# Kernel optimization log

Hardware: AMD Instinct MI355X
Metric: run time of the kernel (lower is better)

## Reference

```python
import jax, jax.numpy as jnp
import numpy as np

B, T, C = 2, 4096, 768
H = 12
D = C // H  # head_dim = 64


def setup_inputs() -> dict:
    key = jax.random.key(0)
    kx, kq, kk, kv, ko = jax.random.split(key, 5)
    s = 1.0 / np.sqrt(C)  # keep activations well-scaled
    return {
        "x": jax.random.normal(kx, (B, T, C), dtype=jnp.float32),
        "wq": jax.random.normal(kq, (C, C), dtype=jnp.float32) * s,
        "wk": jax.random.normal(kk, (C, C), dtype=jnp.float32) * s,
        "wv": jax.random.normal(kv, (C, C), dtype=jnp.float32) * s,
        "wo": jax.random.normal(ko, (C, C), dtype=jnp.float32) * s,
    }


def reference(x, wq, wk, wv, wo):
    b, t, c = x.shape
    # projections (torch Linear: y = x @ W.T); split heads -> (B,H,T,D)
    q = (x @ wq.T).reshape(b, t, H, D).transpose(0, 2, 1, 3)
    k = (x @ wk.T).reshape(b, t, H, D).transpose(0, 2, 1, 3)
    v = (x @ wv.T).reshape(b, t, H, D).transpose(0, 2, 1, 3)
    scale = 1.0 / jnp.sqrt(jnp.asarray(D, dtype=x.dtype))
    scores = jnp.einsum("bhqd,bhkd->bhqk", q, k) * scale  # (B,H,T,T)
    causal = jnp.tril(jnp.ones((t, t), dtype=bool))
    scores = jnp.where(causal, scores, jnp.asarray(-jnp.inf, dtype=scores.dtype))
    attn = jax.nn.softmax(scores, axis=-1)
    ctx = jnp.einsum("bhqk,bhkd->bhqd", attn, v)  # (B,H,T,D)
    ctx = ctx.transpose(0, 2, 1, 3).reshape(b, t, c)
    return ctx @ wo.T
```

## Files before the change

kernel.cpp:

```cpp
#include <hip/hip_runtime.h>
#include <hip/hip_bf16.h>

#define B_  2
#define T_  4096
#define C_  768
#define H_  12
#define D_  64
#define MTOT (B_*T_)

typedef __bf16 bf16;
typedef __bf16 bf16x8 __attribute__((ext_vector_type(8)));
typedef __bf16 bf16x4 __attribute__((ext_vector_type(4)));
typedef float  f32x4  __attribute__((ext_vector_type(4)));

__device__ __forceinline__ void gl_lds16(const bf16* g, bf16* l) {
    __builtin_amdgcn_global_load_lds(
        (const __attribute__((address_space(1))) void*)g,
        (__attribute__((address_space(3))) void*)l, 16, 0, 0);
}

__global__ __launch_bounds__(256) void cvt_bf16(const float* __restrict__ src,
                                                bf16* __restrict__ dst, int n8) {
    int i = blockIdx.x * 256 + threadIdx.x;
    if (i >= n8) return;
    const float4* s4 = (const float4*)src;
    float4 a = s4[2*(size_t)i], b = s4[2*(size_t)i+1];
    bf16x8 o;
    o[0]=(bf16)a.x; o[1]=(bf16)a.y; o[2]=(bf16)a.z; o[3]=(bf16)a.w;
    o[4]=(bf16)b.x; o[5]=(bf16)b.y; o[6]=(bf16)b.z; o[7]=(bf16)b.w;
    *(bf16x8*)(dst + 8*(size_t)i) = o;
}

__global__ __launch_bounds__(256) void cvt_bf16_w4(const float* __restrict__ w0,
                                                   const float* __restrict__ w1,
                                                   const float* __restrict__ w2,
                                                   const float* __restrict__ w3,
                                                   bf16* __restrict__ d0,
                                                   bf16* __restrict__ d1,
                                                   bf16* __restrict__ d2,
                                                   bf16* __restrict__ d3) {
    int z = blockIdx.y;
    const float* src = (z==0)?w0:(z==1)?w1:(z==2)?w2:w3;
    bf16* dst = (z==0)?d0:(z==1)?d1:(z==2)?d2:d3;
    int i = blockIdx.x * 256 + threadIdx.x;
    const float4* s4 = (const float4*)src;
    float4 a = s4[2*(size_t)i], b = s4[2*(size_t)i+1];
    bf16x8 o;
    o[0]=(bf16)a.x; o[1]=(bf16)a.y; o[2]=(bf16)a.z; o[3]=(bf16)a.w;
    o[4]=(bf16)b.x; o[5]=(bf16)b.y; o[6]=(bf16)b.z; o[7]=(bf16)b.w;
    *(bf16x8*)(dst + 8*(size_t)i) = o;
}

__global__ __launch_bounds__(256) void gemm_qkv(const bf16* __restrict__ xb,
                                                const bf16* __restrict__ wqb,
                                                const bf16* __restrict__ wkb,
                                                const bf16* __restrict__ wvb,
                                                bf16* __restrict__ qo,
                                                bf16* __restrict__ ko,
                                                bf16* __restrict__ vto) {
    int z = blockIdx.z;
    const bf16* w = (z == 0) ? wqb : (z == 1) ? wkb : wvb;
    bf16* dst = (z == 0) ? qo : (z == 1) ? ko : vto;
    int mbase = blockIdx.x * 128;
    int nbase = blockIdx.y * 128;
    __shared__ bf16 As[128][32];
    __shared__ bf16 Bs[128][32];
    int tid  = threadIdx.x;
    int wave = tid >> 6, lane = tid & 63;
    int wm = (wave >> 1) * 64, wn = (wave & 1) * 64;
    int lr = lane & 15, lg = lane >> 4;
    int srow0 = tid >> 2, scol0 = tid & 3;
    int srow1 = (tid + 256) >> 2, scol1 = (tid + 256) & 3;
    f32x4 acc[4][4] = {};
    for (int kb = 0; kb < C_; kb += 32) {
        gl_lds16(xb + (size_t)(mbase + srow0) * C_ + kb + scol0 * 8, &As[srow0][scol0 * 8]);
        gl_lds16(xb + (size_t)(mbase + srow1) * C_ + kb + scol1 * 8, &As[srow1][scol1 * 8]);
        gl_lds16(w  + (size_t)(nbase + srow0) * C_ + kb + scol0 * 8, &Bs[srow0][scol0 * 8]);
        gl_lds16(w  + (size_t)(nbase + srow1) * C_ + kb + scol1 * 8, &Bs[srow1][scol1 * 8]);
        __syncthreads();
        bf16x8 af[4], bfr[4];
        #pragma unroll
        for (int mt = 0; mt < 4; ++mt) af[mt]  = *(const bf16x8*)(&As[wm + mt*16 + lr][lg*8]);
        #pragma unroll
        for (int nt = 0; nt < 4; ++nt) bfr[nt] = *(const bf16x8*)(&Bs[wn + nt*16 + lr][lg*8]);
        #pragma unroll
        for (int mt = 0; mt < 4; ++mt)
            #pragma unroll
            for (int nt = 0; nt < 4; ++nt)
                acc[mt][nt] = __builtin_amdgcn_mfma_f32_16x16x32_bf16(af[mt], bfr[nt], acc[mt][nt], 0, 0, 0);
        __syncthreads();
    }
    float sc = (z == 0) ? 0.18033688011112042f : 1.0f;
    int m0 = mbase + wm + (lg << 2);
    int n0 = nbase + wn + lr;
    if (z < 2) {
        #pragma unroll
        for (int mt = 0; mt < 4; ++mt) {
            #pragma unroll
            for (int nt = 0; nt < 4; ++nt) {
                int n = n0 + nt * 16;
                int h = n >> 6, d = n & 63;
                #pragma unroll
                for (int r = 0; r < 4; ++r) {
                    int m = m0 + mt * 16 + r;
                    int b = m >> 12, t = m & 4095;
                    dst[(((size_t)b * H_ + h) * T_ + t) * 64 + d] = (bf16)(acc[mt][nt][r] * sc);
                }
            }
        }
    } else {
        #pragma unroll
        for (int mt = 0; mt < 4; ++mt) {
            int m = m0 + mt * 16;
            int b = m >> 12, t = m & 4095;
            #pragma unroll
            for (int nt = 0; nt < 4; ++nt) {
                int n = n0 + nt * 16;
                int h = n >> 6, d = n & 63;
                bf16x4 pk;
                #pragma unroll
                for (int r = 0; r < 4; ++r) pk[r] = (bf16)acc[mt][nt][r];
                *(bf16x4*)(dst + (((size_t)b * H_ + h) * 64 + d) * T_ + t) = pk;
            }
        }
    }
}

__global__ __launch_bounds__(256) void gemm_out(const bf16* __restrict__ ctx,
                                                const bf16* __restrict__ wob,
                                                float* __restrict__ out) {
    int mbase = blockIdx.x * 128;
    int nbase = blockIdx.y * 128;
    __shared__ bf16 As[128][32];
    __shared__ bf16 Bs[128][32];
    int tid  = threadIdx.x;
    int wave = tid >> 6, lane = tid & 63;
    int wm = (wave >> 1) * 64, wn = (wave & 1) * 64;
    int lr = lane & 15, lg = lane >> 4;
    int srow0 = tid >> 2, scol0 = tid & 3;
    int srow1 = (tid + 256) >> 2, scol1 = (tid + 256) & 3;
    f32x4 acc[4][4] = {};
    for (int kb = 0; kb < C_; kb += 32) {
        gl_lds16(ctx + (size_t)(mbase + srow0) * C_ + kb + scol0 * 8, &As[srow0][scol0 * 8]);
        gl_lds16(ctx + (size_t)(mbase + srow1) * C_ + kb + scol1 * 8, &As[srow1][scol1 * 8]);
        gl_lds16(wob + (size_t)(nbase + srow0) * C_ + kb + scol0 * 8, &Bs[srow0][scol0 * 8]);
        gl_lds16(wob + (size_t)(nbase + srow1) * C_ + kb + scol1 * 8, &Bs[srow1][scol1 * 8]);
        __syncthreads();
        bf16x8 af[4], bfr[4];
        #pragma unroll
        for (int mt = 0; mt < 4; ++mt) af[mt]  = *(const bf16x8*)(&As[wm + mt*16 + lr][lg*8]);
        #pragma unroll
        for (int nt = 0; nt < 4; ++nt) bfr[nt] = *(const bf16x8*)(&Bs[wn + nt*16 + lr][lg*8]);
        #pragma unroll
        for (int mt = 0; mt < 4; ++mt)
            #pragma unroll
            for (int nt = 0; nt < 4; ++nt)
                acc[mt][nt] = __builtin_amdgcn_mfma_f32_16x16x32_bf16(af[mt], bfr[nt], acc[mt][nt], 0, 0, 0);
        __syncthreads();
    }
    int m0 = mbase + wm + (lg << 2);
    int n0 = nbase + wn + lr;
    #pragma unroll
    for (int mt = 0; mt < 4; ++mt)
        #pragma unroll
        for (int nt = 0; nt < 4; ++nt)
            #pragma unroll
            for (int r = 0; r < 4; ++r)
                out[(size_t)(m0 + mt * 16 + r) * C_ + n0 + nt * 16] = acc[mt][nt][r];
}

__global__ __launch_bounds__(256, 4) void attn(const bf16* __restrict__ q,
                                               const bf16* __restrict__ k,
                                               const bf16* __restrict__ vt,
                                               bf16* __restrict__ ctx) {
    int idx = blockIdx.x;
    int qt = 63 - idx / 24;
    int bh = idx % 24;
    int b = bh / H_, h = bh % H_;
    int tid = threadIdx.x;
    int wave = tid >> 6, lane = tid & 63;
    int lr = lane & 15, lg = lane >> 4;

    __shared__ bf16 Ks[64][72];
    __shared__ bf16 Vs[64][72];
    __shared__ bf16 Pb[4][16][72];

    const bf16* qp = q  + (size_t)bh * T_ * 64;
    const bf16* kp = k  + (size_t)bh * T_ * 64;
    const bf16* vp = vt + (size_t)bh * 64 * (size_t)T_;

    int r0 = tid >> 3, c0 = tid & 7;
    const bf16* kstg = kp + (size_t)r0 * 64 + c0 * 8;
    const bf16* vstg = vp + (size_t)r0 * T_ + c0 * 8;

    const float NEGINF = -__builtin_inff();

    int qb = qt * 64 + wave * 16;
    int n  = qt + 1;
    int qrow = qb + lr;

    bf16x8 qf[2];
    #pragma unroll
    for (int c = 0; c < 2; ++c)
        qf[c] = *(const bf16x8*)(qp + (size_t)(qb + lr) * 64 + c * 32 + lg * 8);

    f32x4 o[4] = {};
    float m = NEGINF, l = 0.f;

    uint4 sk0 = *(const uint4*)(kstg);
    uint4 sk1 = *(const uint4*)(kstg + 32 * 64);
    uint4 sv0 = *(const uint4*)(vstg);
    uint4 sv1 = *(const uint4*)(vstg + (size_t)32 * T_);

    for (int kb = 0; kb < n; ++kb) {
        int kv = kb * 64;
        __syncthreads();
        *(uint4*)(&Ks[r0][c0 * 8])      = sk0;
        *(uint4*)(&Ks[32 + r0][c0 * 8]) = sk1;
        *(uint4*)(&Vs[r0][c0 * 8])      = sv0;
        *(uint4*)(&Vs[32 + r0][c0 * 8]) = sv1;
        if (kb + 1 < n) {
            const bf16* ksrc = kstg + (size_t)(kb + 1) * 64 * 64;
            const bf16* vsrc = vstg + (size_t)(kb + 1) * 64;
            sk0 = *(const uint4*)(ksrc);
            sk1 = *(const uint4*)(ksrc + 32 * 64);
            sv0 = *(const uint4*)(vsrc);
            sv1 = *(const uint4*)(vsrc + (size_t)32 * T_);
        }
        __syncthreads();

        f32x4 s[4] = {};
        #pragma unroll
        for (int c2 = 0; c2 < 2; ++c2)
            #pragma unroll
            for (int nt = 0; nt < 4; ++nt) {
                bf16x8 kf = *(const bf16x8*)(&Ks[nt * 16 + lr][c2 * 32 + lg * 8]);
                s[nt] = __builtin_amdgcn_mfma_f32_16x16x32_bf16(kf, qf[c2], s[nt], 0, 0, 0);
            }
        if (kb == qt) {
            #pragma unroll
            for (int nt = 0; nt < 4; ++nt)
                #pragma unroll
                for (int r = 0; r < 4; ++r) {
                    int key = kv + nt * 16 + lg * 4 + r;
                    s[nt][r] = (key > qrow) ? NEGINF : s[nt][r];
                }
        }
        float mx = s[0][0];
        #pragma unroll
        for (int nt = 0; nt < 4; ++nt) {
            float a = fmaxf(s[nt][0], s[nt][1]);
            float bq = fmaxf(s[nt][2], s[nt][3]);
            mx = fmaxf(mx, fmaxf(a, bq));
        }
        mx = fmaxf(mx, __shfl_xor(mx, 16, 64));
        mx = fmaxf(mx, __shfl_xor(mx, 32, 64));
        float mn = fmaxf(m, mx);
        float al = __builtin_amdgcn_exp2f(m - mn);
        m = mn;
        float sm = 0.f;
        #pragma unroll
        for (int nt = 0; nt < 4; ++nt)
            #pragma unroll
            for (int r = 0; r < 4; ++r) {
                float p = __builtin_amdgcn_exp2f(s[nt][r] - mn);
                s[nt][r] = p;
                sm += p;
            }
        sm += __shfl_xor(sm, 16, 64);
        sm += __shfl_xor(sm, 32, 64);
        l = l * al + sm;
        #pragma unroll
        for (int dt = 0; dt < 4; ++dt)
            #pragma unroll
            for (int r = 0; r < 4; ++r) o[dt][r] *= al;
        #pragma unroll
        for (int nt = 0; nt < 4; ++nt) {
            bf16x4 pk;
            #pragma unroll
            for (int r = 0; r < 4; ++r) pk[r] = (bf16)s[nt][r];
            *(bf16x4*)(&Pb[wave][lr][nt * 16 + lg * 4]) = pk;
        }
        #pragma unroll
        for (int c2 = 0; c2 < 2; ++c2) {
            bf16x8 pf = *(const bf16x8*)(&Pb[wave][lr][c2 * 32 + lg * 8]);
            #pragma unroll
            for (int dt = 0; dt < 4; ++dt) {
                bf16x8 vfr = *(const bf16x8*)(&Vs[dt * 16 + lr][c2 * 32 + lg * 8]);
                o[dt] = __builtin_amdgcn_mfma_f32_16x16x32_bf16(vfr, pf, o[dt], 0, 0, 0);
            }
        }
    }

    float inv = 1.0f / l;
    #pragma unroll
    for (int dt = 0; dt < 4; ++dt) {
        bf16x4 pk;
        #pragma unroll
        for (int r = 0; r < 4; ++r) pk[r] = (bf16)(o[dt][r] * inv);
        *(bf16x4*)(ctx + ((size_t)b * T_ + qb + lr) * C_ + h * 64 + dt * 16 + lg * 4) = pk;
    }
}

extern "C" void kernel_launch(void* const* d_in, const int* in_sizes, int n_in,
                              void* d_out, int out_size, void* d_ws, size_t ws_size,
                              hipStream_t stream) {
    const float* x  = (const float*)d_in[0];
    const float* wq = (const float*)d_in[1];
    const float* wk = (const float*)d_in[2];
    const float* wv = (const float*)d_in[3];
    const float* wo = (const float*)d_in[4];
    float* out = (float*)d_out;

    char* ws = (char*)d_ws;
    const size_t SZ_XB = (size_t)MTOT * C_ * sizeof(bf16);
    const size_t SZ_W  = (size_t)C_ * C_ * sizeof(bf16);
    bf16* xb  = (bf16*)(ws);
    bf16* wqb = (bf16*)(ws + SZ_XB);
    bf16* wkb = (bf16*)(ws + SZ_XB + SZ_W);
    bf16* wvb = (bf16*)(ws + SZ_XB + 2 * SZ_W);
    bf16* wob = (bf16*)(ws + SZ_XB + 3 * SZ_W);
    bf16* qb  = (bf16*)(ws + SZ_XB + 4 * SZ_W);
    bf16* kb  = (bf16*)(ws + 2 * SZ_XB + 4 * SZ_W);
    bf16* vtb = (bf16*)(ws + 3 * SZ_XB + 4 * SZ_W);
    bf16* ctb = (bf16*)(ws + 4 * SZ_XB + 4 * SZ_W);

    cvt_bf16<<<3072, 256, 0, stream>>>(x, xb, MTOT * C_ / 8);
    cvt_bf16_w4<<<dim3(288, 4), 256, 0, stream>>>(wq, wk, wv, wo, wqb, wkb, wvb, wob);

    gemm_qkv<<<dim3(MTOT / 128, C_ / 128, 3), 256, 0, stream>>>(xb, wqb, wkb, wvb, qb, kb, vtb);
    attn<<<1536, 256, 0, stream>>>(qb, kb, vtb, ctb);
    gemm_out<<<dim3(MTOT / 128, C_ / 128), 256, 0, stream>>>(ctb, wob, out);
}
```

Measured before the change: 250.8 us.

## Process two 16-row query subtiles per wave in attention, halving block threads

The attention kernel now runs 2 waves per block instead of 4, each wave covering 32 query rows as two 16-row subtiles. Each K and V fragment loaded from LDS feeds two MFMAs, which raises data reuse per LDS read. The block-wide K/V staging loads grow from 2 to 4 per thread because fewer threads share the tile. The cost is more registers per wave (two accumulator sets and two softmax states), fewer waves per block to hide latency, and launch bounds changed to (128,2).

```diff
diff --git a/kernel.cpp b/kernel.cpp
--- a/kernel.cpp
+++ b/kernel.cpp
@@ -169,7 +169,7 @@
                 out[(size_t)(m0 + mt * 16 + r) * C_ + n0 + nt * 16] = acc[mt][nt][r];
 }
 
-__global__ __launch_bounds__(256, 4) void attn(const bf16* __restrict__ q,
+__global__ __launch_bounds__(128, 2) void attn(const bf16* __restrict__ q,
                                                const bf16* __restrict__ k,
                                                const bf16* __restrict__ vt,
                                                bf16* __restrict__ ctx) {
@@ -183,7 +183,7 @@
 
     __shared__ bf16 Ks[64][72];
     __shared__ bf16 Vs[64][72];
-    __shared__ bf16 Pb[4][16][72];
+    __shared__ bf16 Pb[2][32][72];
 
     const bf16* qp = q  + (size_t)bh * T_ * 64;
     const bf16* kp = k  + (size_t)bh * T_ * 64;
@@ -195,110 +195,128 @@
 
     const float NEGINF = -__builtin_inff();
 
-    int qb = qt * 64 + wave * 16;
+    int qb = qt * 64 + wave * 32;
     int n  = qt + 1;
-    int qrow = qb + lr;
-
-    bf16x8 qf[2];
+
+    bf16x8 qf[2][2];
     #pragma unroll
-    for (int c = 0; c < 2; ++c)
-        qf[c] = *(const bf16x8*)(qp + (size_t)(qb + lr) * 64 + c * 32 + lg * 8);
-
-    f32x4 o[4] = {};
-    float m = NEGINF, l = 0.f;
-
-    uint4 sk0 = *(const uint4*)(kstg);
-    uint4 sk1 = *(const uint4*)(kstg + 32 * 64);
-    uint4 sv0 = *(const uint4*)(vstg);
-    uint4 sv1 = *(const uint4*)(vstg + (size_t)32 * T_);
+    for (int qs = 0; qs < 2; ++qs)
+        #pragma unroll
+        for (int c = 0; c < 2; ++c)
+            qf[qs][c] = *(const bf16x8*)(qp + (size_t)(qb + qs * 16 + lr) * 64 + c * 32 + lg * 8);
+
+    f32x4 o[2][4] = {};
+    float mm[2] = {NEGINF, NEGINF}, ll[2] = {0.f, 0.f};
+
+    uint4 sk[4], sv[4];
+    #pragma unroll
+    for (int it = 0; it < 4; ++it) {
+        sk[it] = *(const uint4*)(kstg + (size_t)(it * 16) * 64);
+        sv[it] = *(const uint4*)(vstg + (size_t)(it * 16) * T_);
+    }
 
     for (int kb = 0; kb < n; ++kb) {
         int kv = kb * 64;
         __syncthreads();
-        *(uint4*)(&Ks[r0][c0 * 8])      = sk0;
-        *(uint4*)(&Ks[32 + r0][c0 * 8]) = sk1;
-        *(uint4*)(&Vs[r0][c0 * 8])      = sv0;
-        *(uint4*)(&Vs[32 + r0][c0 * 8]) = sv1;
+        #pragma unroll
+        for (int it = 0; it < 4; ++it) {
+            *(uint4*)(&Ks[r0 + 16 * it][c0 * 8]) = sk[it];
+            *(uint4*)(&Vs[r0 + 16 * it][c0 * 8]) = sv[it];
+        }
         if (kb + 1 < n) {
             const bf16* ksrc = kstg + (size_t)(kb + 1) * 64 * 64;
             const bf16* vsrc = vstg + (size_t)(kb + 1) * 64;
-            sk0 = *(const uint4*)(ksrc);
-            sk1 = *(const uint4*)(ksrc + 32 * 64);
-            sv0 = *(const uint4*)(vsrc);
-            sv1 = *(const uint4*)(vsrc + (size_t)32 * T_);
-        }
-        __syncthreads();
-
-        f32x4 s[4] = {};
+            #pragma unroll
+            for (int it = 0; it < 4; ++it) {
+                sk[it] = *(const uint4*)(ksrc + (size_t)(it * 16) * 64);
+                sv[it] = *(const uint4*)(vsrc + (size_t)(it * 16) * T_);
+            }
+        }
+        __syncthreads();
+
+        f32x4 s[2][4] = {};
         #pragma unroll
         for (int c2 = 0; c2 < 2; ++c2)
             #pragma unroll
             for (int nt = 0; nt < 4; ++nt) {
                 bf16x8 kf = *(const bf16x8*)(&Ks[nt * 16 + lr][c2 * 32 + lg * 8]);
-                s[nt] = __builtin_amdgcn_mfma_f32_16x16x32_bf16(kf, qf[c2], s[nt], 0, 0, 0);
+                s[0][nt] = __builtin_amdgcn_mfma_f32_16x16x32_bf16(kf, qf[0][c2], s[0][nt], 0, 0, 0);
+                s[1][nt] = __builtin_amdgcn_mfma_f32_16x16x32_bf16(kf, qf[1][c2], s[1][nt], 0, 0, 0);
             }
         if (kb == qt) {
             #pragma unroll
+            for (int qs = 0; qs < 2; ++qs) {
+                int qrow = qb + qs * 16 + lr;
+                #pragma unroll
+                for (int nt = 0; nt < 4; ++nt)
+                    #pragma unroll
+                    for (int r = 0; r < 4; ++r) {
+                        int key = kv + nt * 16 + lg * 4 + r;
+                        s[qs][nt][r] = (key > qrow) ? NEGINF : s[qs][nt][r];
+                    }
+            }
+        }
+        #pragma unroll
+        for (int qs = 0; qs < 2; ++qs) {
+            float mx = s[qs][0][0];
+            #pragma unroll
+            for (int nt = 0; nt < 4; ++nt) {
+                float a = fmaxf(s[qs][nt][0], s[qs][nt][1]);
+                float bq = fmaxf(s[qs][nt][2], s[qs][nt][3]);
+                mx = fmaxf(mx, fmaxf(a, bq));
+            }
+            mx = fmaxf(mx, __shfl_xor(mx, 16, 64));
+            mx = fmaxf(mx, __shfl_xor(mx, 32, 64));
+            float mn = fmaxf(mm[qs], mx);
+            float al = __builtin_amdgcn_exp2f(mm[qs] - mn);
+            mm[qs] = mn;
+            float sm = 0.f;
+            #pragma unroll
             for (int nt = 0; nt < 4; ++nt)
                 #pragma unroll
                 for (int r = 0; r < 4; ++r) {
-                    int key = kv + nt * 16 + lg * 4 + r;
-                    s[nt][r] = (key > qrow) ? NEGINF : s[nt][r];
+                    float p = __builtin_amdgcn_exp2f(s[qs][nt][r] - mn);
+                    s[qs][nt][r] = p;
+                    sm += p;
                 }
-        }
-        float mx = s[0][0];
-        #pragma unroll
-        for (int nt = 0; nt < 4; ++nt) {
-            float a = fmaxf(s[nt][0], s[nt][1]);
-            float bq = fmaxf(s[nt][2], s[nt][3]);
-            mx = fmaxf(mx, fmaxf(a, bq));
-        }
-        mx = fmaxf(mx, __shfl_xor(mx, 16, 64));
-        mx = fmaxf(mx, __shfl_xor(mx, 32, 64));
-        float mn = fmaxf(m, mx);
-        float al = __builtin_amdgcn_exp2f(m - mn);
-        m = mn;
-        float sm = 0.f;
-        #pragma unroll
-        for (int nt = 0; nt < 4; ++nt)
-            #pragma unroll
-            for (int r = 0; r < 4; ++r) {
-                float p = __builtin_amdgcn_exp2f(s[nt][r] - mn);
-                s[nt][r] = p;
-                sm += p;
-            }
-        sm += __shfl_xor(sm, 16, 64);
-        sm += __shfl_xor(sm, 32, 64);
-        l = l * al + sm;
-        #pragma unroll
-        for (int dt = 0; dt < 4; ++dt)
-            #pragma unroll
-            for (int r = 0; r < 4; ++r) o[dt][r] *= al;
-        #pragma unroll
-        for (int nt = 0; nt < 4; ++nt) {
-            bf16x4 pk;
-            #pragma unroll
-            for (int r = 0; r < 4; ++r) pk[r] = (bf16)s[nt][r];
-            *(bf16x4*)(&Pb[wave][lr][nt * 16 + lg * 4]) = pk;
+            sm += __shfl_xor(sm, 16, 64);
+            sm += __shfl_xor(sm, 32, 64);
+            ll[qs] = ll[qs] * al + sm;
+            #pragma unroll
+            for (int dt = 0; dt < 4; ++dt)
+                #pragma unroll
+                for (int r = 0; r < 4; ++r) o[qs][dt][r] *= al;
+            #pragma unroll
+            for (int nt = 0; nt < 4; ++nt) {
+                bf16x4 pk;
+                #pragma unroll
+                for (int r = 0; r < 4; ++r) pk[r] = (bf16)s[qs][nt][r];
+                *(bf16x4*)(&Pb[wave][qs * 16 + lr][nt * 16 + lg * 4]) = pk;
+            }
         }
         #pragma unroll
         for (int c2 = 0; c2 < 2; ++c2) {
-            bf16x8 pf = *(const bf16x8*)(&Pb[wave][lr][c2 * 32 + lg * 8]);
+            bf16x8 pf0 = *(const bf16x8*)(&Pb[wave][lr][c2 * 32 + lg * 8]);
+            bf16x8 pf1 = *(const bf16x8*)(&Pb[wave][16 + lr][c2 * 32 + lg * 8]);
             #pragma unroll
             for (int dt = 0; dt < 4; ++dt) {
                 bf16x8 vfr = *(const bf16x8*)(&Vs[dt * 16 + lr][c2 * 32 + lg * 8]);
-                o[dt] = __builtin_amdgcn_mfma_f32_16x16x32_bf16(vfr, pf, o[dt], 0, 0, 0);
-            }
-        }
-    }
-
-    float inv = 1.0f / l;
+                o[0][dt] = __builtin_amdgcn_mfma_f32_16x16x32_bf16(vfr, pf0, o[0][dt], 0, 0, 0);
+                o[1][dt] = __builtin_amdgcn_mfma_f32_16x16x32_bf16(vfr, pf1, o[1][dt], 0, 0, 0);
+            }
+        }
+    }
+
     #pragma unroll
-    for (int dt = 0; dt < 4; ++dt) {
-        bf16x4 pk;
-        #pragma unroll
-        for (int r = 0; r < 4; ++r) pk[r] = (bf16)(o[dt][r] * inv);
-        *(bf16x4*)(ctx + ((size_t)b * T_ + qb + lr) * C_ + h * 64 + dt * 16 + lg * 4) = pk;
+    for (int qs = 0; qs < 2; ++qs) {
+        float inv = 1.0f / ll[qs];
+        #pragma unroll
+        for (int dt = 0; dt < 4; ++dt) {
+            bf16x4 pk;
+            #pragma unroll
+            for (int r = 0; r < 4; ++r) pk[r] = (bf16)(o[qs][dt][r] * inv);
+            *(bf16x4*)(ctx + ((size_t)b * T_ + qb + qs * 16 + lr) * C_ + h * 64 + dt * 16 + lg * 4) = pk;
+        }
     }
 }
 
@@ -329,6 +347,6 @@
     cvt_bf16_w4<<<dim3(288, 4), 256, 0, stream>>>(wq, wk, wv, wo, wqb, wkb, wvb, wob);
 
     gemm_qkv<<<dim3(MTOT / 128, C_ / 128, 3), 256, 0, stream>>>(xb, wqb, wkb, wvb, qb, kb, vtb);
-    attn<<<1536, 256, 0, stream>>>(qb, kb, vtb, ctb);
+    attn<<<1536, 128, 0, stream>>>(qb, kb, vtb, ctb);
     gemm_out<<<dim3(MTOT / 128, C_ / 128), 256, 0, stream>>>(ctb, wob, out);
 }
```

After: 400.5 us. 1.6x slower.
